# Kernel optimization log

Hardware: AMD Instinct MI355X
Metric: run time of the kernel (lower is better)

## Reference

```python
import jax, jax.numpy as jnp
import numpy as np

NUM_INPUTS = 376
NUM_ACTIONS = 17
L1, L2 = 256, 128
BHID = 128
NE = 2
B = 65536


def setup_inputs() -> dict:
    key = jax.random.key(0)
    ks = jax.random.split(key, 16)
    s = lambda k, shape: jax.random.normal(k, shape, dtype=jnp.float32) * 0.05
    return {
        "states": jax.random.normal(ks[0], (B, NUM_INPUTS), dtype=jnp.float32),
        # blending module params
        "bw1": s(ks[1], (BHID, NUM_INPUTS)), "bb1": s(ks[2], (BHID,)),
        "bw2": s(ks[3], (BHID, BHID)),       "bb2": s(ks[4], (BHID,)),
        "bwo": s(ks[5], (NE, BHID)),         "bbo": s(ks[6], (NE,)),
        # stacked expert (p1, p2) policy params, leading axis = expert
        "ew1": s(ks[7], (NE, L1, NUM_INPUTS)), "eb1": s(ks[8], (NE, L1)),
        "ew2": s(ks[9], (NE, L2, L1)),         "eb2": s(ks[10], (NE, L2)),
        "ewm": s(ks[11], (NE, NUM_ACTIONS, L2)), "ebm": s(ks[12], (NE, NUM_ACTIONS)),
    }


def _blended_linear(h, coeffs, W, b):
    # Linear with per-sample blended weights: (sum_e c_e W_e) h + sum_e c_e b_e
    # == sum_e c_e (W_e h + b_e), so compute both expert outputs and blend.
    y = jnp.einsum('bi,eoi->beo', h, W) + b[None]  # [B, E, O]
    return jnp.einsum('be,beo->bo', coeffs, y)


def reference(states, bw1, bb1, bw2, bb2, bwo, bbo, ew1, eb1, ew2, eb2, ewm, ebm):
    # BlendingModule: 2-layer relu MLP -> softmax over experts
    g = jax.nn.relu(states @ bw1.T + bb1)
    g = jax.nn.relu(g @ bw2.T + bb2)
    coeffs = jax.nn.softmax(g @ bwo.T + bbo, axis=-1)  # [B, 2]
    # Per-sample blended PolicyModule (256 -> 128 -> actions, tanh head)
    h = jax.nn.relu(_blended_linear(states, coeffs, ew1, eb1))
    h = jax.nn.relu(_blended_linear(h, coeffs, ew2, eb2))
    mu = jnp.tanh(_blended_linear(h, coeffs, ewm, ebm))
    return mu
```

## Files before the change

### kernel.cpp

```cpp
#include <hip/hip_runtime.h>
#include <math.h>


typedef __attribute__((ext_vector_type(8))) _Float16 half8;
typedef __attribute__((ext_vector_type(4))) _Float16 half4;
typedef __attribute__((ext_vector_type(4))) float    f32x4;

#define MFMA16(a, b, c) __builtin_amdgcn_mfma_f32_16x16x32_f16((a), (b), (c), 0, 0, 0)
#define SWZ(row) (((row) & 7) << 4)

#define MT 32
#define T  512

#define S_B      0
#define G1_B     24576
#define G2_B     32768
#define H1_B     24576
#define H2_B     24576
#define LDS_BYTES 40960

#define WS_W1 0
#define WS_W2 49152
#define WS_E1 65536
#define WS_E2 262144
#define WS_EM 327680
#define WS_HALFS 335872
#define WS_BYTES 671744

__device__ __forceinline__ half8 cvt8(const float* __restrict__ p) {
    const float4 a = *reinterpret_cast<const float4*>(p);
    const float4 b = *reinterpret_cast<const float4*>(p + 4);
    half8 r;
    r[0] = (_Float16)a.x; r[1] = (_Float16)a.y; r[2] = (_Float16)a.z; r[3] = (_Float16)a.w;
    r[4] = (_Float16)b.x; r[5] = (_Float16)b.y; r[6] = (_Float16)b.z; r[7] = (_Float16)b.w;
    return r;
}

__global__ __launch_bounds__(256)
void prep_weights(const float* __restrict__ bw1, const float* __restrict__ bw2,
                  const float* __restrict__ ew1, const float* __restrict__ ew2,
                  const float* __restrict__ ewm, _Float16* __restrict__ wsw)
{
    const int i = blockIdx.x * 256 + threadIdx.x;
    if (i >= WS_HALFS) return;
    const float* W; int N, K, KC, j0;
    if      (i < 49152)  { W = bw1; N = 128; K = 376; KC = 12; j0 = i - WS_W1; }
    else if (i < 65536)  { W = bw2; N = 128; K = 128; KC = 4;  j0 = i - WS_W2; }
    else if (i < 262144) { W = ew1; N = 512; K = 376; KC = 12; j0 = i - WS_E1; }
    else if (i < 327680) { W = ew2; N = 256; K = 256; KC = 8;  j0 = i - WS_E2; }
    else                 { W = ewm; N = 34;  K = 128; KC = 4;  j0 = i - WS_EM; }
    const int tile = j0 >> 9;
    const int rem  = j0 & 511;
    const int l    = rem >> 3;
    const int jj   = rem & 7;
    const int n0   = tile / KC, kc = tile - n0 * KC;
    int n = n0 * 16 + (l & 15);
    const int k = kc * 32 + (l >> 4) * 8 + jj;
    float v = 0.f;
    if (W == ewm) {
        const int e = n >> 5, a = n & 31;
        if (a < 17 && k < K) v = ewm[(e * 17 + a) * K + k];
    } else {
        if (n < N && k < K) v = W[n * K + k];
    }
    wsw[i] = (_Float16)v;
}

template <bool USE_WS>
__global__ __launch_bounds__(512)
__attribute__((amdgpu_waves_per_eu(2)))
void actor_kernel(const float* __restrict__ states,
                  const float* __restrict__ bw1, const float* __restrict__ bb1,
                  const float* __restrict__ bw2, const float* __restrict__ bb2,
                  const float* __restrict__ bwo, const float* __restrict__ bbo,
                  const float* __restrict__ ew1, const float* __restrict__ eb1,
                  const float* __restrict__ ew2, const float* __restrict__ eb2,
                  const float* __restrict__ ewm, const float* __restrict__ ebm,
                  const _Float16* __restrict__ wsw,
                  float* __restrict__ out)
{
    extern __shared__ char smc[];
    const int t    = threadIdx.x;
    const int l    = t & 63;
    const int l15  = l & 15;
    const int kgrp = l >> 4;
    const int kg16 = kgrp * 16;
    const int wv   = __builtin_amdgcn_readfirstlane(t >> 6);
    const int base = blockIdx.x * MT;
    const int lB   = l * 8;

    const half8 zf = {0,0,0,0,0,0,0,0};

    {
        const float4* src = reinterpret_cast<const float4*>(states + (long)base * 376);
        for (int q = t; q < MT * 94; q += T) {
            const int r  = q / 94;
            const int c4 = q - r * 94;
            const float4 v = src[q];
            half4 h;
            h[0] = (_Float16)v.x; h[1] = (_Float16)v.y;
            h[2] = (_Float16)v.z; h[3] = (_Float16)v.w;
            *(half4*)(smc + S_B + ((r * 768 + c4 * 8) ^ SWZ(r))) = h;
        }
        if (t < MT) {
            *(float4*)(smc + S_B + ((t * 768 + 752) ^ SWZ(t))) = make_float4(0.f, 0.f, 0.f, 0.f);
        }
    }
    __syncthreads();

    {
        f32x4 acc[2] = {{0,0,0,0},{0,0,0,0}};
        const int col = wv * 16 + l15;
        auto ldW = [&](int kc) -> half8 {
            if constexpr (USE_WS) return *(const half8*)(wsw + WS_W1 + (wv * 12 + kc) * 512 + lB);
            else { const int g = kc * 4 + kgrp; return (g < 47) ? cvt8(bw1 + col * 376 + g * 8) : zf; }
        };
        half8 bf = ldW(0);
        #pragma unroll
        for (int kc = 0; kc < 12; ++kc) {
            const half8 cur = bf;
            if (kc < 11) bf = ldW(kc + 1);
            const int koff = kc * 64 + kg16;
            #pragma unroll
            for (int mt = 0; mt < 2; ++mt) {
                const int row = mt * 16 + l15;
                const half8 af = *(const half8*)(smc + S_B + ((row * 768 + koff) ^ SWZ(row)));
                acc[mt] = MFMA16(af, cur, acc[mt]);
            }
        }
        const float bias = bb1[col];
        #pragma unroll
        for (int mt = 0; mt < 2; ++mt) {
            #pragma unroll
            for (int j = 0; j < 4; ++j) {
                const int row = mt * 16 + kgrp * 4 + j;
                const float v = fmaxf(acc[mt][j] + bias, 0.f);
                *(_Float16*)(smc + G1_B + ((row * 256 + col * 2) ^ SWZ(row))) = (_Float16)v;
            }
        }
    }
    __syncthreads();

    {
        f32x4 acc[2] = {{0,0,0,0},{0,0,0,0}};
        const int col = wv * 16 + l15;
        auto ldW = [&](int kc) -> half8 {
            if constexpr (USE_WS) return *(const half8*)(wsw + WS_W2 + (wv * 4 + kc) * 512 + lB);
            else                  return cvt8(bw2 + col * 128 + (kc * 4 + kgrp) * 8);
        };
        half8 bf = ldW(0);
        #pragma unroll
        for (int kc = 0; kc < 4; ++kc) {
            const half8 cur = bf;
            if (kc < 3) bf = ldW(kc + 1);
            const int koff = kc * 64 + kg16;
            #pragma unroll
            for (int mt = 0; mt < 2; ++mt) {
                const int row = mt * 16 + l15;
                const half8 af = *(const half8*)(smc + G1_B + ((row * 256 + koff) ^ SWZ(row)));
                acc[mt] = MFMA16(af, cur, acc[mt]);
            }
        }
        const float bias = bb2[col];
        #pragma unroll
        for (int mt = 0; mt < 2; ++mt) {
            #pragma unroll
            for (int j = 0; j < 4; ++j) {
                const int row = mt * 16 + kgrp * 4 + j;
                const float v = fmaxf(acc[mt][j] + bias, 0.f);
                *(_Float16*)(smc + G2_B + ((row * 256 + col * 2) ^ SWZ(row))) = (_Float16)v;
            }
        }
    }
    __syncthreads();

    {
        const int s     = t >> 4;
        const int r     = t & 15;
        const int e     = r & 1;
        const int chunk = r >> 1;
        float z = 0.f;
        const float* wo = bwo + e * 128 + chunk * 16;
        #pragma unroll
        for (int q = 0; q < 2; ++q) {
            const half8 hv = *(const half8*)(smc + G2_B + ((s * 256 + chunk * 32 + q * 16) ^ SWZ(s)));
            const float4 w0 = *(const float4*)(wo + q * 8);
            const float4 w1 = *(const float4*)(wo + q * 8 + 4);
            z = fmaf((float)hv[0], w0.x, z); z = fmaf((float)hv[1], w0.y, z);
            z = fmaf((float)hv[2], w0.z, z); z = fmaf((float)hv[3], w0.w, z);
            z = fmaf((float)hv[4], w1.x, z); z = fmaf((float)hv[5], w1.y, z);
            z = fmaf((float)hv[6], w1.z, z); z = fmaf((float)hv[7], w1.w, z);
        }
        z += __shfl_xor(z, 2, 64);
        z += __shfl_xor(z, 4, 64);
        z += __shfl_xor(z, 8, 64);
        z += bbo[e];
        const float zo = __shfl_xor(z, 1, 64);
        if (r < 2) {
            const float m = fmaxf(z, zo);
            const float ea = __expf(z - m), eb = __expf(zo - m);
            const float c_self = ea / (ea + eb);
            const _Float16 ch = (_Float16)c_self;
            const _Float16 cl = (_Float16)(c_self - (float)ch);
            union { _Float16 h[2]; unsigned u; } pk;
            pk.h[0] = ch; pk.h[1] = cl;
            *(unsigned*)(smc + S_B + (((s * 768 + 752) ^ SWZ(s)) + e * 4)) = pk.u;
        }
    }
    __syncthreads();

    {
        f32x4 aA[2][2], aB[2][2];
        #pragma unroll
        for (int nt = 0; nt < 2; ++nt)
            #pragma unroll
            for (int mt = 0; mt < 2; ++mt) { aA[nt][mt] = {0,0,0,0}; aB[nt][mt] = {0,0,0,0}; }

        auto ldE1 = [&](int kc, int nt, int ex) -> half8 {
            if constexpr (USE_WS) {
                const int n0 = wv * 2 + nt + ex * 16;
                return *(const half8*)(wsw + WS_E1 + (n0 * 12 + kc) * 512 + lB);
            } else {
                const int g = kc * 4 + kgrp;
                const int wr = wv * 32 + nt * 16 + l15 + ex * 256;
                return (g < 47) ? cvt8(ew1 + wr * 376 + g * 8) : zf;
            }
        };
        half8 b00 = ldE1(0, 0, 0), b01 = ldE1(0, 0, 1);
        half8 b10 = ldE1(0, 1, 0), b11 = ldE1(0, 1, 1);
        #pragma unroll
        for (int kc = 0; kc < 12; ++kc) {
            const half8 c00 = b00, c01 = b01, c10 = b10, c11 = b11;
            if (kc < 11) {
                b00 = ldE1(kc + 1, 0, 0); b01 = ldE1(kc + 1, 0, 1);
                b10 = ldE1(kc + 1, 1, 0); b11 = ldE1(kc + 1, 1, 1);
            }
            const int koff = kc * 64 + kg16;
            #pragma unroll
            for (int mt = 0; mt < 2; ++mt) {
                const int row = mt * 16 + l15;
                const half8 af = *(const half8*)(smc + S_B + ((row * 768 + koff) ^ SWZ(row)));
                aA[0][mt] = MFMA16(af, c00, aA[0][mt]);
                aB[0][mt] = MFMA16(af, c01, aB[0][mt]);
                aA[1][mt] = MFMA16(af, c10, aA[1][mt]);
                aB[1][mt] = MFMA16(af, c11, aB[1][mt]);
            }
        }
        #pragma unroll
        for (int nt = 0; nt < 2; ++nt) {
            const int col = wv * 32 + nt * 16 + l15;
            const float b0 = eb1[col], b1 = eb1[256 + col];
            #pragma unroll
            for (int mt = 0; mt < 2; ++mt) {
                #pragma unroll
                for (int j = 0; j < 4; ++j) {
                    const int row = mt * 16 + kgrp * 4 + j;
                    const half4 cc = *(const half4*)(smc + S_B + ((row * 768 + 752) ^ SWZ(row)));
                    const float c0 = (float)cc[0] + (float)cc[1];
                    const float c1 = (float)cc[2] + (float)cc[3];
                    float v = c0 * (aA[nt][mt][j] + b0) + c1 * (aB[nt][mt][j] + b1);
                    v = fmaxf(v, 0.f);
                    *(_Float16*)(smc + H1_B + ((row * 512 + col * 2) ^ SWZ(row))) = (_Float16)v;
                }
            }
        }
    }
    __syncthreads();

    {
        f32x4 cA[2], cB[2];
        #pragma unroll
        for (int mt = 0; mt < 2; ++mt) { cA[mt] = {0,0,0,0}; cB[mt] = {0,0,0,0}; }
        const int col = wv * 16 + l15;
        auto ldE2 = [&](int kc, int ex) -> half8 {
            if constexpr (USE_WS) {
                return *(const half8*)(wsw + WS_E2 + ((wv + ex * 8) * 8 + kc) * 512 + lB);
            } else {
                const int g = kc * 4 + kgrp;
                return cvt8(ew2 + (col + ex * 128) * 256 + g * 8);
            }
        };
        half8 b0 = ldE2(0, 0), b1 = ldE2(0, 1);
        #pragma unroll
        for (int kc = 0; kc < 8; ++kc) {
            const half8 c0f = b0, c1f = b1;
            if (kc < 7) { b0 = ldE2(kc + 1, 0); b1 = ldE2(kc + 1, 1); }
            const int koff = kc * 64 + kg16;
            #pragma unroll
            for (int mt = 0; mt < 2; ++mt) {
                const int row = mt * 16 + l15;
                const half8 af = *(const half8*)(smc + H1_B + ((row * 512 + koff) ^ SWZ(row)));
                cA[mt] = MFMA16(af, c0f, cA[mt]);
                cB[mt] = MFMA16(af, c1f, cB[mt]);
            }
        }
        __syncthreads();
        const float b0s = eb2[col], b1s = eb2[128 + col];
        #pragma unroll
        for (int mt = 0; mt < 2; ++mt) {
            #pragma unroll
            for (int j = 0; j < 4; ++j) {
                const int row = mt * 16 + kgrp * 4 + j;
                const half4 cc = *(const half4*)(smc + S_B + ((row * 768 + 752) ^ SWZ(row)));
                const float c0 = (float)cc[0] + (float)cc[1];
                const float c1 = (float)cc[2] + (float)cc[3];
                float v = c0 * (cA[mt][j] + b0s) + c1 * (cB[mt][j] + b1s);
                v = fmaxf(v, 0.f);
                *(_Float16*)(smc + H2_B + ((row * 256 + col * 2) ^ SWZ(row))) = (_Float16)v;
            }
        }
    }
    __syncthreads();

    if (wv < 4) {
        const int colt = wv & 1;
        const int mt   = wv >> 1;
        f32x4 c0a = {0,0,0,0}, c1a = {0,0,0,0};
        const int col  = colt * 16 + l15;
        const bool vcol = (col < 17);
        const int arow = mt * 16 + l15;
        for (int kc = 0; kc < 4; ++kc) {
            const int koff = kc * 64 + kg16;
            const half8 af = *(const half8*)(smc + H2_B + ((arow * 256 + koff) ^ SWZ(arow)));
            half8 b0, b1;
            if constexpr (USE_WS) {
                b0 = *(const half8*)(wsw + WS_EM + (colt * 4 + kc) * 512 + lB);
                b1 = *(const half8*)(wsw + WS_EM + ((2 + colt) * 4 + kc) * 512 + lB);
            } else {
                const int g = kc * 4 + kgrp;
                b0 = vcol ? cvt8(ewm + col * 128 + g * 8)        : zf;
                b1 = vcol ? cvt8(ewm + (17 + col) * 128 + g * 8) : zf;
            }
            c0a = MFMA16(af, b0, c0a);
            c1a = MFMA16(af, b1, c1a);
        }
        if (vcol) {
            const float b0 = ebm[col], b1 = ebm[17 + col];
            #pragma unroll
            for (int j = 0; j < 4; ++j) {
                const int row = mt * 16 + kgrp * 4 + j;
                const half4 cc = *(const half4*)(smc + S_B + ((row * 768 + 752) ^ SWZ(row)));
                const float c0 = (float)cc[0] + (float)cc[1];
                const float c1 = (float)cc[2] + (float)cc[3];
                const float v = c0 * (c0a[j] + b0) + c1 * (c1a[j] + b1);
                out[(long)(base + row) * 17 + col] = tanhf(v);
            }
        }
    }
}

extern "C" void kernel_launch(void* const* d_in, const int* in_sizes, int n_in,
                              void* d_out, int out_size, void* d_ws, size_t ws_size,
                              hipStream_t stream) {
    (void)in_sizes; (void)n_in; (void)out_size;
    const float* states = (const float*)d_in[0];
    const float* bw1 = (const float*)d_in[1];
    const float* bb1 = (const float*)d_in[2];
    const float* bw2 = (const float*)d_in[3];
    const float* bb2 = (const float*)d_in[4];
    const float* bwo = (const float*)d_in[5];
    const float* bbo = (const float*)d_in[6];
    const float* ew1 = (const float*)d_in[7];
    const float* eb1 = (const float*)d_in[8];
    const float* ew2 = (const float*)d_in[9];
    const float* eb2 = (const float*)d_in[10];
    const float* ewm = (const float*)d_in[11];
    const float* ebm = (const float*)d_in[12];
    float* out = (float*)d_out;

    const int nblk = 65536 / MT;

    if (d_ws != nullptr && ws_size >= (size_t)WS_BYTES) {
        _Float16* wsw = (_Float16*)d_ws;
        prep_weights<<<dim3((WS_HALFS + 255) / 256), dim3(256), 0, stream>>>(
            bw1, bw2, ew1, ew2, ewm, wsw);
        actor_kernel<true><<<dim3(nblk), dim3(T), LDS_BYTES, stream>>>(
            states, bw1, bb1, bw2, bb2, bwo, bbo,
            ew1, eb1, ew2, eb2, ewm, ebm, wsw, out);
    } else {
        actor_kernel<false><<<dim3(nblk), dim3(T), LDS_BYTES, stream>>>(
            states, bw1, bb1, bw2, bb2, bwo, bbo,
            ew1, eb1, ew2, eb2, ewm, ebm, nullptr, out);
    }
}
```

Before: 86.82 us.

## Prefetch weights two steps ahead and across layer boundaries

Weight fragments are now double-buffered two k-steps ahead instead of one. The first fragments of each following layer are issued before the epilogue and barrier of the current layer, so global-load latency overlaps the syncs and bias/ReLU writes. The head layer's loop is also unrolled with prefetching. This raises register pressure, which may reduce occupancy.

```diff
diff --git a/kernel.cpp b/kernel.cpp
--- a/kernel.cpp
+++ b/kernel.cpp
@@ -91,6 +91,36 @@
 
     const half8 zf = {0,0,0,0,0,0,0,0};
 
+    const int colA = wv * 16 + l15;
+    auto ldW1 = [&](int kc) -> half8 {
+        if constexpr (USE_WS) return *(const half8*)(wsw + WS_W1 + (wv * 12 + kc) * 512 + lB);
+        else { const int g = kc * 4 + kgrp; return (g < 47) ? cvt8(bw1 + colA * 376 + g * 8) : zf; }
+    };
+    auto ldW2 = [&](int kc) -> half8 {
+        if constexpr (USE_WS) return *(const half8*)(wsw + WS_W2 + (wv * 4 + kc) * 512 + lB);
+        else                  return cvt8(bw2 + colA * 128 + (kc * 4 + kgrp) * 8);
+    };
+    auto ldE1 = [&](int kc, int nt, int ex) -> half8 {
+        if constexpr (USE_WS) {
+            const int n0 = wv * 2 + nt + ex * 16;
+            return *(const half8*)(wsw + WS_E1 + (n0 * 12 + kc) * 512 + lB);
+        } else {
+            const int g = kc * 4 + kgrp;
+            const int wr = wv * 32 + nt * 16 + l15 + ex * 256;
+            return (g < 47) ? cvt8(ew1 + wr * 376 + g * 8) : zf;
+        }
+    };
+    auto ldE2 = [&](int kc, int ex) -> half8 {
+        if constexpr (USE_WS) {
+            return *(const half8*)(wsw + WS_E2 + ((wv + ex * 8) * 8 + kc) * 512 + lB);
+        } else {
+            const int g = kc * 4 + kgrp;
+            return cvt8(ew2 + (colA + ex * 128) * 256 + g * 8);
+        }
+    };
+
+    half8 w0 = ldW1(0), w1 = ldW1(1);
+
     {
         const float4* src = reinterpret_cast<const float4*>(states + (long)base * 376);
         for (int q = t; q < MT * 94; q += T) {
@@ -108,18 +138,13 @@
     }
     __syncthreads();
 
+    half8 n0a, n0b;
     {
         f32x4 acc[2] = {{0,0,0,0},{0,0,0,0}};
-        const int col = wv * 16 + l15;
-        auto ldW = [&](int kc) -> half8 {
-            if constexpr (USE_WS) return *(const half8*)(wsw + WS_W1 + (wv * 12 + kc) * 512 + lB);
-            else { const int g = kc * 4 + kgrp; return (g < 47) ? cvt8(bw1 + col * 376 + g * 8) : zf; }
-        };
-        half8 bf = ldW(0);
         #pragma unroll
         for (int kc = 0; kc < 12; ++kc) {
-            const half8 cur = bf;
-            if (kc < 11) bf = ldW(kc + 1);
+            const half8 cur = (kc & 1) ? w1 : w0;
+            if (kc + 2 < 12) { if (kc & 1) w1 = ldW1(kc + 2); else w0 = ldW1(kc + 2); }
             const int koff = kc * 64 + kg16;
             #pragma unroll
             for (int mt = 0; mt < 2; ++mt) {
@@ -128,31 +153,28 @@
                 acc[mt] = MFMA16(af, cur, acc[mt]);
             }
         }
-        const float bias = bb1[col];
+        n0a = ldW2(0); n0b = ldW2(1);
+        const float bias = bb1[colA];
         #pragma unroll
         for (int mt = 0; mt < 2; ++mt) {
             #pragma unroll
             for (int j = 0; j < 4; ++j) {
                 const int row = mt * 16 + kgrp * 4 + j;
                 const float v = fmaxf(acc[mt][j] + bias, 0.f);
-                *(_Float16*)(smc + G1_B + ((row * 256 + col * 2) ^ SWZ(row))) = (_Float16)v;
-            }
-        }
-    }
-    __syncthreads();
-
+                *(_Float16*)(smc + G1_B + ((row * 256 + colA * 2) ^ SWZ(row))) = (_Float16)v;
+            }
+        }
+    }
+    __syncthreads();
+
+    half8 e1q[2][4];
     {
         f32x4 acc[2] = {{0,0,0,0},{0,0,0,0}};
-        const int col = wv * 16 + l15;
-        auto ldW = [&](int kc) -> half8 {
-            if constexpr (USE_WS) return *(const half8*)(wsw + WS_W2 + (wv * 4 + kc) * 512 + lB);
-            else                  return cvt8(bw2 + col * 128 + (kc * 4 + kgrp) * 8);
-        };
-        half8 bf = ldW(0);
+        w0 = n0a; w1 = n0b;
         #pragma unroll
         for (int kc = 0; kc < 4; ++kc) {
-            const half8 cur = bf;
-            if (kc < 3) bf = ldW(kc + 1);
+            const half8 cur = (kc & 1) ? w1 : w0;
+            if (kc + 2 < 4) { if (kc & 1) w1 = ldW2(kc + 2); else w0 = ldW2(kc + 2); }
             const int koff = kc * 64 + kg16;
             #pragma unroll
             for (int mt = 0; mt < 2; ++mt) {
@@ -161,14 +183,18 @@
                 acc[mt] = MFMA16(af, cur, acc[mt]);
             }
         }
-        const float bias = bb2[col];
+        e1q[0][0] = ldE1(0, 0, 0); e1q[0][1] = ldE1(0, 0, 1);
+        e1q[0][2] = ldE1(0, 1, 0); e1q[0][3] = ldE1(0, 1, 1);
+        e1q[1][0] = ldE1(1, 0, 0); e1q[1][1] = ldE1(1, 0, 1);
+        e1q[1][2] = ldE1(1, 1, 0); e1q[1][3] = ldE1(1, 1, 1);
+        const float bias = bb2[colA];
         #pragma unroll
         for (int mt = 0; mt < 2; ++mt) {
             #pragma unroll
             for (int j = 0; j < 4; ++j) {
                 const int row = mt * 16 + kgrp * 4 + j;
                 const float v = fmaxf(acc[mt][j] + bias, 0.f);
-                *(_Float16*)(smc + G2_B + ((row * 256 + col * 2) ^ SWZ(row))) = (_Float16)v;
+                *(_Float16*)(smc + G2_B + ((row * 256 + colA * 2) ^ SWZ(row))) = (_Float16)v;
             }
         }
     }
@@ -184,12 +210,12 @@
         #pragma unroll
         for (int q = 0; q < 2; ++q) {
             const half8 hv = *(const half8*)(smc + G2_B + ((s * 256 + chunk * 32 + q * 16) ^ SWZ(s)));
-            const float4 w0 = *(const float4*)(wo + q * 8);
-            const float4 w1 = *(const float4*)(wo + q * 8 + 4);
-            z = fmaf((float)hv[0], w0.x, z); z = fmaf((float)hv[1], w0.y, z);
-            z = fmaf((float)hv[2], w0.z, z); z = fmaf((float)hv[3], w0.w, z);
-            z = fmaf((float)hv[4], w1.x, z); z = fmaf((float)hv[5], w1.y, z);
-            z = fmaf((float)hv[6], w1.z, z); z = fmaf((float)hv[7], w1.w, z);
+            const float4 wv0 = *(const float4*)(wo + q * 8);
+            const float4 wv1 = *(const float4*)(wo + q * 8 + 4);
+            z = fmaf((float)hv[0], wv0.x, z); z = fmaf((float)hv[1], wv0.y, z);
+            z = fmaf((float)hv[2], wv0.z, z); z = fmaf((float)hv[3], wv0.w, z);
+            z = fmaf((float)hv[4], wv1.x, z); z = fmaf((float)hv[5], wv1.y, z);
+            z = fmaf((float)hv[6], wv1.z, z); z = fmaf((float)hv[7], wv1.w, z);
         }
         z += __shfl_xor(z, 2, 64);
         z += __shfl_xor(z, 4, 64);
@@ -209,6 +235,7 @@
     }
     __syncthreads();
 
+    half8 e2q[2][2];
     {
         f32x4 aA[2][2], aB[2][2];
         #pragma unroll
@@ -216,24 +243,13 @@
             #pragma unroll
             for (int mt = 0; mt < 2; ++mt) { aA[nt][mt] = {0,0,0,0}; aB[nt][mt] = {0,0,0,0}; }
 
-        auto ldE1 = [&](int kc, int nt, int ex) -> half8 {
-            if constexpr (USE_WS) {
-                const int n0 = wv * 2 + nt + ex * 16;
-                return *(const half8*)(wsw + WS_E1 + (n0 * 12 + kc) * 512 + lB);
-            } else {
-                const int g = kc * 4 + kgrp;
-                const int wr = wv * 32 + nt * 16 + l15 + ex * 256;
-                return (g < 47) ? cvt8(ew1 + wr * 376 + g * 8) : zf;
-            }
-        };
-        half8 b00 = ldE1(0, 0, 0), b01 = ldE1(0, 0, 1);
-        half8 b10 = ldE1(0, 1, 0), b11 = ldE1(0, 1, 1);
         #pragma unroll
         for (int kc = 0; kc < 12; ++kc) {
-            const half8 c00 = b00, c01 = b01, c10 = b10, c11 = b11;
-            if (kc < 11) {
-                b00 = ldE1(kc + 1, 0, 0); b01 = ldE1(kc + 1, 0, 1);
-                b10 = ldE1(kc + 1, 1, 0); b11 = ldE1(kc + 1, 1, 1);
+            const int d = kc & 1;
+            const half8 c00 = e1q[d][0], c01 = e1q[d][1], c10 = e1q[d][2], c11 = e1q[d][3];
+            if (kc + 2 < 12) {
+                e1q[d][0] = ldE1(kc + 2, 0, 0); e1q[d][1] = ldE1(kc + 2, 0, 1);
+                e1q[d][2] = ldE1(kc + 2, 1, 0); e1q[d][3] = ldE1(kc + 2, 1, 1);
             }
             const int koff = kc * 64 + kg16;
             #pragma unroll
@@ -246,6 +262,8 @@
                 aB[1][mt] = MFMA16(af, c11, aB[1][mt]);
             }
         }
+        e2q[0][0] = ldE2(0, 0); e2q[0][1] = ldE2(0, 1);
+        e2q[1][0] = ldE2(1, 0); e2q[1][1] = ldE2(1, 1);
         #pragma unroll
         for (int nt = 0; nt < 2; ++nt) {
             const int col = wv * 32 + nt * 16 + l15;
@@ -267,24 +285,16 @@
     }
     __syncthreads();
 
+    half8 e3a, e3b;
     {
         f32x4 cA[2], cB[2];
         #pragma unroll
         for (int mt = 0; mt < 2; ++mt) { cA[mt] = {0,0,0,0}; cB[mt] = {0,0,0,0}; }
-        const int col = wv * 16 + l15;
-        auto ldE2 = [&](int kc, int ex) -> half8 {
-            if constexpr (USE_WS) {
-                return *(const half8*)(wsw + WS_E2 + ((wv + ex * 8) * 8 + kc) * 512 + lB);
-            } else {
-                const int g = kc * 4 + kgrp;
-                return cvt8(ew2 + (col + ex * 128) * 256 + g * 8);
-            }
-        };
-        half8 b0 = ldE2(0, 0), b1 = ldE2(0, 1);
         #pragma unroll
         for (int kc = 0; kc < 8; ++kc) {
-            const half8 c0f = b0, c1f = b1;
-            if (kc < 7) { b0 = ldE2(kc + 1, 0); b1 = ldE2(kc + 1, 1); }
+            const int d = kc & 1;
+            const half8 c0f = e2q[d][0], c1f = e2q[d][1];
+            if (kc + 2 < 8) { e2q[d][0] = ldE2(kc + 2, 0); e2q[d][1] = ldE2(kc + 2, 1); }
             const int koff = kc * 64 + kg16;
             #pragma unroll
             for (int mt = 0; mt < 2; ++mt) {
@@ -294,8 +304,19 @@
                 cB[mt] = MFMA16(af, c1f, cB[mt]);
             }
         }
+        {
+            const int colt = wv & 1;
+            if constexpr (USE_WS) {
+                e3a = *(const half8*)(wsw + WS_EM + (colt * 4 + 0) * 512 + lB);
+                e3b = *(const half8*)(wsw + WS_EM + ((2 + colt) * 4 + 0) * 512 + lB);
+            } else {
+                const int col = colt * 16 + l15;
+                e3a = (col < 17) ? cvt8(ewm + col * 128 + kgrp * 8)        : zf;
+                e3b = (col < 17) ? cvt8(ewm + (17 + col) * 128 + kgrp * 8) : zf;
+            }
+        }
         __syncthreads();
-        const float b0s = eb2[col], b1s = eb2[128 + col];
+        const float b0s = eb2[colA], b1s = eb2[128 + colA];
         #pragma unroll
         for (int mt = 0; mt < 2; ++mt) {
             #pragma unroll
@@ -306,7 +327,7 @@
                 const float c1 = (float)cc[2] + (float)cc[3];
                 float v = c0 * (cA[mt][j] + b0s) + c1 * (cB[mt][j] + b1s);
                 v = fmaxf(v, 0.f);
-                *(_Float16*)(smc + H2_B + ((row * 256 + col * 2) ^ SWZ(row))) = (_Float16)v;
+                *(_Float16*)(smc + H2_B + ((row * 256 + colA * 2) ^ SWZ(row))) = (_Float16)v;
             }
         }
     }
@@ -319,18 +340,22 @@
         const int col  = colt * 16 + l15;
         const bool vcol = (col < 17);
         const int arow = mt * 16 + l15;
+        half8 pb0 = e3a, pb1 = e3b;
+        #pragma unroll
         for (int kc = 0; kc < 4; ++kc) {
+            const half8 b0 = pb0, b1 = pb1;
+            if (kc + 1 < 4) {
+                if constexpr (USE_WS) {
+                    pb0 = *(const half8*)(wsw + WS_EM + (colt * 4 + kc + 1) * 512 + lB);
+                    pb1 = *(const half8*)(wsw + WS_EM + ((2 + colt) * 4 + kc + 1) * 512 + lB);
+                } else {
+                    const int g = (kc + 1) * 4 + kgrp;
+                    pb0 = vcol ? cvt8(ewm + col * 128 + g * 8)        : zf;
+                    pb1 = vcol ? cvt8(ewm + (17 + col) * 128 + g * 8) : zf;
+                }
+            }
             const int koff = kc * 64 + kg16;
             const half8 af = *(const half8*)(smc + H2_B + ((arow * 256 + koff) ^ SWZ(arow)));
-            half8 b0, b1;
-            if constexpr (USE_WS) {
-                b0 = *(const half8*)(wsw + WS_EM + (colt * 4 + kc) * 512 + lB);
-                b1 = *(const half8*)(wsw + WS_EM + ((2 + colt) * 4 + kc) * 512 + lB);
-            } else {
-                const int g = kc * 4 + kgrp;
-                b0 = vcol ? cvt8(ewm + col * 128 + g * 8)        : zf;
-                b1 = vcol ? cvt8(ewm + (17 + col) * 128 + g * 8) : zf;
-            }
             c0a = MFMA16(af, b0, c0a);
             c1a = MFMA16(af, b1, c1a);
         }
```

After: 96.88 us. 1.12x slower.
